# Performance work log

Measured on AMD Instinct MI355X. Metric: run time of the kernel, lower is better.

## Reference

```python
import jax, jax.numpy as jnp
import numpy as np

B, N, DIM, H = 4, 3072, 768, 3  # N must be 48*64 per positional-encoding assert; H must be 3 per reshape constraint
HD = DIM // H               # 256
D = HD + 6                  # per-head dim after positional concat


def _positional(n):
    # (x^2, y^2, xy, x, y, 1) encoding over a 48x64 grid, intrinsics=None path.
    h, w = 48, 64
    ys = jnp.linspace(-1.0, 1.0, h)
    xs = jnp.linspace(-1.0, 1.0, w)
    p3 = jnp.tile(ys, w)            # [N], ys.unsqueeze(0).repeat(B, w)
    p4 = jnp.repeat(xs, h)          # [N], xs.repeat_interleave(h)
    pos = jnp.stack([p3 * p3, p4 * p4, p3 * p4, p3, p4, jnp.ones_like(p3)], axis=-1)  # [N,6]
    return pos


def setup_inputs() -> dict:
    key = jax.random.key(0)
    k0, k1, k2 = jax.random.split(key, 3)
    x = jax.random.normal(k0, (B, N, DIM), dtype=jnp.float32)
    W_qkv = jax.random.normal(k1, (3 * DIM, DIM), dtype=jnp.float32) * (DIM ** -0.5)
    W_pf = jax.random.normal(k2, (DIM, DIM + 6 * H), dtype=jnp.float32) * ((DIM + 6 * H) ** -0.5)
    b_pf = jnp.zeros((DIM,), dtype=jnp.float32)
    return {"x": x, "W_qkv": W_qkv, "W_pf": W_pf, "b_pf": b_pf}


def reference(x, W_qkv, W_pf, b_pf):
    Bb, Nn, C = x.shape
    scale = HD ** -0.5
    qkv = (x @ W_qkv.T).reshape(Bb, Nn, 3, H, HD).transpose(2, 0, 3, 1, 4)  # [3,B,H,N,hd]
    q, k, v = qkv[0], qkv[1], qkv[2]
    attn = jnp.einsum('bhnd,bhmd->bhnm', q, k) * scale          # [B,H,N,N]
    attn_f = jax.nn.softmax(attn, axis=-1) * jax.nn.softmax(attn, axis=-2)
    pos = _positional(Nn)                                       # [N,6]
    pos_b = jnp.broadcast_to(pos[None, None], (Bb, H, Nn, 6))
    v_cat = jnp.concatenate([v, pos_b], axis=-1)                # [B,H,N,D]
    # fundamental = v^T @ attn_f @ v  -> [B,H,D,D]
    f1 = jnp.einsum('bhnd,bhnm->bhdm', v_cat, attn_f)
    fund = jnp.einsum('bhdm,bhme->bhde', f1, v_cat)
    # reshape [B,H,D,D] -> [B, 3D, D] -> transpose -> [B, D, 3D]
    fund = fund.reshape(Bb, H * D, D).transpose(0, 2, 1)
    out = fund @ W_pf.T + b_pf                                  # [B, D, DIM]
    return out
```

## Files before the change

### kernel.cpp

```cpp
#include <hip/hip_runtime.h>

typedef unsigned short u16;
typedef u16 u16x8 __attribute__((ext_vector_type(8)));
typedef u16 u16x4 __attribute__((ext_vector_type(4)));
typedef __bf16 bf16x8 __attribute__((ext_vector_type(8)));
typedef float f32x4 __attribute__((ext_vector_type(4)));

#define Bn   4
#define Nn   3072
#define DIMn 768
#define Hn   3
#define HDn  256
#define BHn  12
#define Dn   262
#define EP   272
#define MSn  8
#define FP   264
#define KSn  4

__device__ __forceinline__ u16 f2bf(float f) {
    unsigned u = __builtin_bit_cast(unsigned, f);
    u += 0x7fffu + ((u >> 16) & 1u);
    return (u16)(u >> 16);
}
__device__ __forceinline__ float bf2f(u16 h) {
    unsigned u = ((unsigned)h) << 16;
    return __builtin_bit_cast(float, u);
}
__device__ __forceinline__ bf16x8 ld_frag16(const u16* p) {
    return *(const bf16x8*)p;
}
#define MFMA(a,b,c) __builtin_amdgcn_mfma_f32_16x16x32_bf16(a, b, c, 0, 0, 0)

__global__ void to_bf16(const float* __restrict__ in, u16* __restrict__ out, int n8) {
    int i = blockIdx.x * blockDim.x + threadIdx.x;
    if (i >= n8) return;
    float4 a = *(const float4*)(in + (size_t)i*8);
    float4 b = *(const float4*)(in + (size_t)i*8 + 4);
    u16x8 o;
    o[0]=f2bf(a.x); o[1]=f2bf(a.y); o[2]=f2bf(a.z); o[3]=f2bf(a.w);
    o[4]=f2bf(b.x); o[5]=f2bf(b.y); o[6]=f2bf(b.z); o[7]=f2bf(b.w);
    *(u16x8*)(out + (size_t)i*8) = o;
}

__global__ __launch_bounds__(256) void transpose_wpf(const float* __restrict__ Wpf,
                                                     float* __restrict__ WpfT) {
    __shared__ float tile[32][33];
    int jt = blockIdx.x * 32;
    int ot = blockIdx.y * 32;
    int tx = threadIdx.x & 31, ty = threadIdx.x >> 5;
    #pragma unroll
    for (int k = 0; k < 4; ++k) {
        int o = ot + ty + 8*k;
        int j = jt + tx;
        tile[ty + 8*k][tx] = (j < 786) ? Wpf[(size_t)o*786 + j] : 0.0f;
    }
    __syncthreads();
    #pragma unroll
    for (int k = 0; k < 4; ++k) {
        int j = jt + ty + 8*k;
        if (j < 786) WpfT[(size_t)j*768 + ot + tx] = tile[tx][ty + 8*k];
    }
}

__global__ __launch_bounds__(256) void qkv_mfma(const u16* __restrict__ xb,
                                                const u16* __restrict__ Wb,
                                                u16* __restrict__ qh,
                                                u16* __restrict__ kh,
                                                u16* __restrict__ vT) {
    __shared__ u16 Pool[2*128*72];
    u16* Xs = Pool;
    u16* Ws = Pool + 128*72;
    int tid = threadIdx.x;
    int w = tid >> 6, lane = tid & 63, quad = lane >> 4, l15 = lane & 15;
    int lid = blockIdx.x + 18*blockIdx.y;
    int swz = (lid & 7)*216 + (lid >> 3);
    int cb = swz % 18, rb = swz / 18;
    int r0 = rb * 128;
    int b_ = rb / 24;
    int n0 = (rb % 24) * 128;
    int which = cb / 6;
    int c0l = (cb % 6) * 128;
    int h = c0l >> 8, hd0 = c0l & 255;
    int bh = b_ * Hn + h;
    int wr = w >> 1, wc = w & 1;
    const u16* xp = xb + (size_t)r0*DIMn;
    const u16* wp = Wb + (size_t)(which*768 + c0l)*DIMn;
    const int sr = tid >> 3, ssg = tid & 7;

    u16x8 xreg[4], wreg[4];
    #pragma unroll
    for (int i = 0; i < 4; ++i) {
        xreg[i] = *(const u16x8*)(xp + (size_t)(sr + 32*i)*DIMn + ssg*8);
        wreg[i] = *(const u16x8*)(wp + (size_t)(sr + 32*i)*DIMn + ssg*8);
    }

    f32x4 acc[4][4];
    #pragma unroll
    for (int i = 0; i < 4; ++i)
        #pragma unroll
        for (int j = 0; j < 4; ++j) acc[i][j] = (f32x4){0.f,0.f,0.f,0.f};

    for (int k0 = 0; k0 < DIMn; k0 += 64) {
        int k0n = (k0 + 64 < DIMn) ? k0 + 64 : 0;
        __syncthreads();
        #pragma unroll
        for (int i = 0; i < 4; ++i) {
            *(u16x8*)&Xs[(sr + 32*i)*72 + ssg*8] = xreg[i];
            *(u16x8*)&Ws[(sr + 32*i)*72 + ssg*8] = wreg[i];
        }
        __syncthreads();
        #pragma unroll
        for (int i = 0; i < 4; ++i) {
            xreg[i] = *(const u16x8*)(xp + (size_t)(sr + 32*i)*DIMn + k0n + ssg*8);
            wreg[i] = *(const u16x8*)(wp + (size_t)(sr + 32*i)*DIMn + k0n + ssg*8);
        }
        #pragma unroll
        for (int ks = 0; ks < 2; ++ks) {
            bf16x8 af[4], bf[4];
            #pragma unroll
            for (int mt = 0; mt < 4; ++mt)
                af[mt] = ld_frag16(&Xs[(wr*64 + mt*16 + l15)*72 + ks*32 + quad*8]);
            #pragma unroll
            for (int nt = 0; nt < 4; ++nt)
                bf[nt] = ld_frag16(&Ws[(wc*64 + nt*16 + l15)*72 + ks*32 + quad*8]);
            #pragma unroll
            for (int mt = 0; mt < 4; ++mt)
                #pragma unroll
                for (int nt = 0; nt < 4; ++nt)
                    acc[mt][nt] = MFMA(af[mt], bf[nt], acc[mt][nt]);
        }
    }
    __syncthreads();
    u16* Cw = Pool + w*(64*72);
    if (which < 2) {
        #pragma unroll
        for (int mt = 0; mt < 4; ++mt)
            #pragma unroll
            for (int nt = 0; nt < 4; ++nt)
                #pragma unroll
                for (int r = 0; r < 4; ++r)
                    Cw[(mt*16 + quad*4 + r)*72 + nt*16 + l15] = f2bf(acc[mt][nt][r]);
    } else {
        #pragma unroll
        for (int mt = 0; mt < 4; ++mt)
            #pragma unroll
            for (int nt = 0; nt < 4; ++nt) {
                u16x4 pk;
                #pragma unroll
                for (int r = 0; r < 4; ++r) pk[r] = f2bf(acc[mt][nt][r]);
                *(u16x4*)&Cw[(nt*16 + l15)*72 + mt*16 + quad*4] = pk;
            }
    }
    __syncthreads();
    #pragma unroll
    for (int i = 0; i < 8; ++i) {
        int u = tid + i*256;
        int row = u >> 4, seg = u & 15;
        if (which < 2) {
            int wv = ((row >> 6) << 1) | (seg >> 3);
            u16x8 vv = *(const u16x8*)&Pool[wv*(64*72) + (row & 63)*72 + (seg & 7)*8];
            u16* dst = (which == 0) ? qh : kh;
            *(u16x8*)(dst + ((size_t)bh*Nn + n0 + row)*HDn + hd0 + seg*8) = vv;
        } else {
            int wv = ((seg >> 3) << 1) | (row >> 6);
            u16x8 vv = *(const u16x8*)&Pool[wv*(64*72) + (row & 63)*72 + (seg & 7)*8];
            *(u16x8*)(vT + ((size_t)bh*EP + hd0 + row)*Nn + n0 + seg*8) = vv;
        }
    }
}

__global__ void pos_fill(u16* __restrict__ vT) {
    int idx = blockIdx.x * blockDim.x + threadIdx.x;
    int bh = idx / (16*Nn);
    int rem = idx - bh*16*Nn;
    int row = rem / Nn;
    int n = rem - row*Nn;
    int gy = n % 48, gx = n / 48;
    float p3 = -1.0f + (2.0f/47.0f)*gy;
    float p4 = -1.0f + (2.0f/63.0f)*gx;
    float v = 0.f;
    if (row == 0) v = p3*p3;
    else if (row == 1) v = p4*p4;
    else if (row == 2) v = p3*p4;
    else if (row == 3) v = p3;
    else if (row == 4) v = p4;
    else if (row == 5) v = 1.0f;
    vT[((size_t)bh*EP + 256 + row)*Nn + n] = f2bf(v);
}

__global__ __launch_bounds__(256) void rc_mfma(const u16* __restrict__ qh,
                                               const u16* __restrict__ kh,
                                               float* __restrict__ R_part,
                                               float* __restrict__ C_part,
                                               u16* __restrict__ P2,
                                               int g0) {
    __shared__ u16 Ks[64*264];
    __shared__ float rbuf[2][2][64];
    int tid = threadIdx.x;
    int w = tid >> 6, lane = tid & 63, quad = lane >> 4, l15 = lane & 15;
    int nwg = (int)(gridDim.x * gridDim.y * gridDim.z);
    int lid = blockIdx.x + (int)gridDim.x*(blockIdx.y + (int)gridDim.y*blockIdx.z);
    int swz = (lid & 7)*(nwg >> 3) + (lid >> 3);
    int ms = swz % MSn;
    int rem_ = swz / MSn;
    int nb = rem_ % 48;
    int bhl = rem_ / 48;
    int bh = g0 + bhl;
    int n0 = nb * 64;
    int msBase = ms * (Nn/MSn);
    const u16* qp = qh + ((size_t)bh*Nn + n0)*HDn;
    const u16* kp = kh + (size_t)bh*Nn*HDn;
    u16* pw = P2 + (size_t)bhl*Nn*Nn;
    int wm = w & 1, wn = w >> 1;

    #pragma unroll
    for (int i = 0; i < 8; ++i) {
        int e = tid + i*256;
        int row = e >> 5, seg = e & 31;
        *(u16x8*)&Ks[row*264 + seg*8] = *(const u16x8*)(qp + (size_t)row*HDn + seg*8);
    }
    __syncthreads();
    bf16x8 qf[2][8];
    #pragma unroll
    for (int nt = 0; nt < 2; ++nt)
        #pragma unroll
        for (int ks = 0; ks < 8; ++ks)
            qf[nt][ks] = ld_frag16(&Ks[((2*wn+nt)*16 + l15)*264 + ks*32 + quad*8]);

    const int kr = tid >> 5, ksg = tid & 31;
    u16x8 kreg[8];
    #pragma unroll
    for (int i = 0; i < 8; ++i)
        kreg[i] = *(const u16x8*)(kp + (size_t)(msBase + kr + 8*i)*HDn + ksg*8);

    float* cpart = C_part + ((size_t)(nb*2 + wn)*BHn + bh)*Nn;
    float rAcc[2] = {0.f, 0.f};
    const int NCH = Nn/(MSn*64);
    for (int mc = 0; mc < NCH; ++mc) {
        int m0 = msBase + mc*64;
        int m0n = msBase + ((mc + 1 < NCH) ? (mc + 1)*64 : 0);
        __syncthreads();
        #pragma unroll
        for (int i = 0; i < 8; ++i)
            *(u16x8*)&Ks[(kr + 8*i)*264 + ksg*8] = kreg[i];
        __syncthreads();
        #pragma unroll
        for (int i = 0; i < 8; ++i)
            kreg[i] = *(const u16x8*)(kp + (size_t)(m0n + kr + 8*i)*HDn + ksg*8);
        f32x4 sacc[2][2];
        #pragma unroll
        for (int i = 0; i < 2; ++i)
            #pragma unroll
            for (int j = 0; j < 2; ++j) sacc[i][j] = (f32x4){0.f,0.f,0.f,0.f};
        #pragma unroll
        for (int ks = 0; ks < 8; ++ks) {
            bf16x8 a0 = ld_frag16(&Ks[((2*wm+0)*16 + l15)*264 + ks*32 + quad*8]);
            bf16x8 a1 = ld_frag16(&Ks[((2*wm+1)*16 + l15)*264 + ks*32 + quad*8]);
            sacc[0][0] = MFMA(a0, qf[0][ks], sacc[0][0]);
            sacc[0][1] = MFMA(a0, qf[1][ks], sacc[0][1]);
            sacc[1][0] = MFMA(a1, qf[0][ks], sacc[1][0]);
            sacc[1][1] = MFMA(a1, qf[1][ks], sacc[1][1]);
        }
        float ex[2][2][4];
        #pragma unroll
        for (int mt = 0; mt < 2; ++mt)
            #pragma unroll
            for (int nt = 0; nt < 2; ++nt)
                #pragma unroll
                for (int r = 0; r < 4; ++r)
                    ex[mt][nt][r] = __expf(0.0625f * sacc[mt][nt][r]);
        #pragma unroll
        for (int mt = 0; mt < 2; ++mt)
            #pragma unroll
            for (int nt = 0; nt < 2; ++nt) {
                u16x4 pk;
                #pragma unroll
                for (int r = 0; r < 4; ++r) {
                    float e2 = ex[mt][nt][r];
                    pk[r] = f2bf(e2 * e2);
                }
                *(u16x4*)(pw + (size_t)(n0 + (2*wn+nt)*16 + l15)*Nn
                             + m0 + (2*wm+mt)*16 + quad*4) = pk;
            }
        #pragma unroll
        for (int nt = 0; nt < 2; ++nt)
            #pragma unroll
            for (int mt = 0; mt < 2; ++mt)
                #pragma unroll
                for (int r = 0; r < 4; ++r) rAcc[nt] += ex[mt][nt][r];
        {
            float v0 = ex[0][0][0] + ex[0][1][0];
            float v1 = ex[0][0][1] + ex[0][1][1];
            float v2 = ex[0][0][2] + ex[0][1][2];
            float v3 = ex[0][0][3] + ex[0][1][3];
            float v4 = ex[1][0][0] + ex[1][1][0];
            float v5 = ex[1][0][1] + ex[1][1][1];
            float v6 = ex[1][0][2] + ex[1][1][2];
            float v7 = ex[1][0][3] + ex[1][1][3];
            int b0 = l15 & 1, b1 = l15 & 2, b2 = l15 & 4;
            float u01 = (b0 ? v1 : v0) + __shfl_xor(b0 ? v0 : v1, 1, 16);
            float u23 = (b0 ? v3 : v2) + __shfl_xor(b0 ? v2 : v3, 1, 16);
            float u45 = (b0 ? v5 : v4) + __shfl_xor(b0 ? v4 : v5, 1, 16);
            float u67 = (b0 ? v7 : v6) + __shfl_xor(b0 ? v6 : v7, 1, 16);
            float t03 = (b1 ? u23 : u01) + __shfl_xor(b1 ? u01 : u23, 2, 16);
            float t47 = (b1 ? u67 : u45) + __shfl_xor(b1 ? u45 : u67, 2, 16);
            float s07 = (b2 ? t47 : t03) + __shfl_xor(b2 ? t03 : t47, 4, 16);
            s07 += __shfl_xor(s07, 8, 16);
            if (l15 < 8)
                cpart[m0 + (2*wm + (l15 >> 2))*16 + quad*4 + (l15 & 3)] = s07;
        }
    }
    #pragma unroll
    for (int nt = 0; nt < 2; ++nt) {
        float rp = rAcc[nt];
        rp += __shfl_xor(rp, 16, 64);
        rp += __shfl_xor(rp, 32, 64);
        if (quad == 0) rbuf[wm][nt][wn*32 + l15] = rp;
    }
    __syncthreads();
    #pragma unroll
    for (int nt = 0; nt < 2; ++nt) {
        if (quad == 0 && wm == 0) {
            float tot = rbuf[0][nt][wn*32 + l15] + rbuf[1][nt][wn*32 + l15];
            R_part[(size_t)ms*BHn*Nn + (size_t)bh*Nn + n0 + (2*wn+nt)*16 + l15] = tot;
        }
    }
}

__global__ void inv_kernel(const float* __restrict__ Rg,
                           const float* __restrict__ Cg,
                           float* __restrict__ iRg, float* __restrict__ iCg) {
    int i = blockIdx.x * blockDim.x + threadIdx.x;
    float r = 0.f;
    #pragma unroll
    for (int s = 0; s < MSn; ++s)
        r += Rg[(size_t)s*BHn*Nn + i];
    float c = 0.f;
    for (int s = 0; s < 96; ++s)
        c += Cg[(size_t)s*BHn*Nn + i];
    iRg[i] = 1.0f / r;
    iCg[i] = 1.0f / c;
}

__global__ void scale_v(const u16* __restrict__ vTg, const float* __restrict__ iCg,
                        u16* __restrict__ vTs) {
    int idx = blockIdx.x * blockDim.x + threadIdx.x;
    int bhl = idx / (EP*Nn/8);
    int rem = idx - bhl*(EP*Nn/8);
    size_t off = (size_t)bhl*EP*Nn + (size_t)rem*8;
    int m = (rem % (Nn/8)) * 8;
    u16x8 v = *(const u16x8*)(vTg + off);
    float4 c0 = *(const float4*)(iCg + (size_t)bhl*Nn + m);
    float4 c1 = *(const float4*)(iCg + (size_t)bhl*Nn + m + 4);
    u16x8 o;
    o[0]=f2bf(bf2f(v[0])*c0.x); o[1]=f2bf(bf2f(v[1])*c0.y);
    o[2]=f2bf(bf2f(v[2])*c0.z); o[3]=f2bf(bf2f(v[3])*c0.w);
    o[4]=f2bf(bf2f(v[4])*c1.x); o[5]=f2bf(bf2f(v[5])*c1.y);
    o[6]=f2bf(bf2f(v[6])*c1.z); o[7]=f2bf(bf2f(v[7])*c1.w);
    *(u16x8*)(vTs + off) = o;
}

__global__ __launch_bounds__(256, 4) void pv_mfma(const u16* __restrict__ P2,
                                                  const u16* __restrict__ vTs,
                                                  const float* __restrict__ iRg,
                                                  u16* __restrict__ f1aTg) {
    __shared__ u16 Ps2[64*72];
    __shared__ u16 Vt[144*72];
    int tid = threadIdx.x;
    int w = tid >> 6, lane = tid & 63, quad = lane >> 4, l15 = lane & 15;
    int nwg = (int)(gridDim.x * gridDim.y * gridDim.z);
    int lid = blockIdx.x + (int)gridDim.x*(blockIdx.y + (int)gridDim.y*blockIdx.z);
    int swz = (lid & 7)*(nwg >> 3) + (lid >> 3);
    int n0b = swz % 48;
    int rem_ = swz / 48;
    int bhl = rem_ % (int)gridDim.y;
    int z = rem_ / (int)gridDim.y;
    int n0 = n0b * 64;
    const u16* pp = P2  + ((size_t)bhl*Nn + n0)*Nn;
    const u16* vp = vTs + (size_t)bhl*EP*Nn + (size_t)(z*128)*Nn;
    const int sr = tid >> 3, sg = tid & 7;
    u16x8 preg[2], vreg[5];
    #pragma unroll
    for (int i = 0; i < 2; ++i)
        preg[i] = *(const u16x8*)(pp + (size_t)(sr + 32*i)*Nn + sg*8);
    #pragma unroll
    for (int i = 0; i < 5; ++i)
        if (i < 4 || (z == 1 && tid < 128))
            vreg[i] = *(const u16x8*)(vp + (size_t)(sr + 32*i)*Nn + sg*8);

    f32x4 acc[4][3];
    #pragma unroll
    for (int a = 0; a < 4; ++a)
        #pragma unroll
        for (int b = 0; b < 3; ++b) acc[a][b] = (f32x4){0.f,0.f,0.f,0.f};

    for (int mc = 0; mc < Nn/64; ++mc) {
        int m0n = (mc + 1 < Nn/64) ? (mc + 1)*64 : 0;
        __syncthreads();
        #pragma unroll
        for (int i = 0; i < 2; ++i)
            *(u16x8*)&Ps2[(sr + 32*i)*72 + sg*8] = preg[i];
        #pragma unroll
        for (int i = 0; i < 5; ++i)
            if (i < 4 || (z == 1 && tid < 128))
                *(u16x8*)&Vt[(sr + 32*i)*72 + sg*8] = vreg[i];
        __syncthreads();
        #pragma unroll
        for (int i = 0; i < 2; ++i)
            preg[i] = *(const u16x8*)(pp + (size_t)(sr + 32*i)*Nn + m0n + sg*8);
        #pragma unroll
        for (int i = 0; i < 5; ++i)
            if (i < 4 || (z == 1 && tid < 128))
                vreg[i] = *(const u16x8*)(vp + (size_t)(sr + 32*i)*Nn + m0n + sg*8);
        #pragma unroll
        for (int ks = 0; ks < 2; ++ks) {
            bf16x8 pa[4];
            #pragma unroll
            for (int nt = 0; nt < 4; ++nt)
                pa[nt] = ld_frag16(&Ps2[(nt*16 + l15)*72 + ks*32 + quad*8]);
            #pragma unroll
            for (int et = 0; et < 3; ++et) {
                const int lt = (et < 2) ? (w*2 + et) : 8;
                const bool act = (et < 2 || (z == 1 && w == 3));
                if (act) {
                    bf16x8 vb = ld_frag16(&Vt[(lt*16 + l15)*72 + ks*32 + quad*8]);
                    #pragma unroll
                    for (int nt = 0; nt < 4; ++nt)
                        acc[nt][et] = MFMA(pa[nt], vb, acc[nt][et]);
                }
            }
        }
    }
    #pragma unroll
    for (int nt = 0; nt < 4; ++nt) {
        float4 ir4 = *(const float4*)(iRg + (size_t)bhl*Nn + n0 + nt*16 + quad*4);
        #pragma unroll
        for (int et = 0; et < 3; ++et) {
            const int tile = (et < 2) ? (z*8 + w*2 + et) : 16;
            const bool act = (et < 2 || (z == 1 && w == 3));
            if (act) {
                int e = tile*16 + l15;
                u16x4 ov;
                #pragma unroll
                for (int r = 0; r < 4; ++r)
                    ov[r] = f2bf(acc[nt][et][r] * ((const float*)&ir4)[r]);
                *(u16x4*)(f1aTg + ((size_t)bhl*EP + e)*Nn + n0 + nt*16 + quad*4) = ov;
            }
        }
    }
}

__global__ __launch_bounds__(256) void fund_mfma(const u16* __restrict__ vT,
                                                 const u16* __restrict__ f1aT,
                                                 float* __restrict__ fund_part) {
    __shared__ u16 At[64*136];
    __shared__ u16 Bt[64*136];
    int tid = threadIdx.x;
    int w = tid >> 6, lane = tid & 63, quad = lane >> 4, l15 = lane & 15;
    int lid = blockIdx.x + 5*(blockIdx.y + 5*blockIdx.z);
    int swz = (lid & 7)*150 + (lid >> 3);
    int ex_ = swz % 5;
    int rem_ = swz / 5;
    int dx_ = rem_ % 5;
    int bz = rem_ / 5;
    int bh = bz >> 2;
    int ks = bz & 3;
    int d0 = dx_ * 64, e0 = ex_ * 64;
    const u16* ap = vT   + (size_t)bh*EP*Nn;
    const u16* bp = f1aT + (size_t)bh*EP*Nn;
    int wd = w & 1, we = w >> 1;
    const u16x8 zero8 = {0,0,0,0,0,0,0,0};
    const int nc0 = ks * (Nn/KSn);
    const int NCH = (Nn/KSn)/128;

    const int srow = tid >> 4, seg = tid & 15;
    u16x8 areg[4], breg[4];
    #pragma unroll
    for (int i = 0; i < 4; ++i) {
        int row = srow + 16*i;
        int da = d0 + row, eb = e0 + row;
        areg[i] = (da < EP) ? *(const u16x8*)(ap + (size_t)da*Nn + nc0 + seg*8) : zero8;
        breg[i] = (eb < EP) ? *(const u16x8*)(bp + (size_t)eb*Nn + nc0 + seg*8) : zero8;
    }

    f32x4 acc[2][2];
    #pragma unroll
    for (int i = 0; i < 2; ++i)
        #pragma unroll
        for (int j = 0; j < 2; ++j) acc[i][j] = (f32x4){0.f,0.f,0.f,0.f};

    for (int mc = 0; mc < NCH; ++mc) {
        int ncn = nc0 + ((mc + 1 < NCH) ? (mc + 1)*128 : 0);
        __syncthreads();
        #pragma unroll
        for (int i = 0; i < 4; ++i) {
            int row = srow + 16*i;
            *(u16x8*)&At[row*136 + seg*8] = areg[i];
            *(u16x8*)&Bt[row*136 + seg*8] = breg[i];
        }
        __syncthreads();
        #pragma unroll
        for (int i = 0; i < 4; ++i) {
            int row = srow + 16*i;
            int da = d0 + row, eb = e0 + row;
            areg[i] = (da < EP) ? *(const u16x8*)(ap + (size_t)da*Nn + ncn + seg*8) : zero8;
            breg[i] = (eb < EP) ? *(const u16x8*)(bp + (size_t)eb*Nn + ncn + seg*8) : zero8;
        }
        #pragma unroll
        for (int kk = 0; kk < 4; ++kk) {
            bf16x8 a0 = ld_frag16(&At[((2*wd+0)*16 + l15)*136 + kk*32 + quad*8]);
            bf16x8 a1 = ld_frag16(&At[((2*wd+1)*16 + l15)*136 + kk*32 + quad*8]);
            bf16x8 b0 = ld_frag16(&Bt[((2*we+0)*16 + l15)*136 + kk*32 + quad*8]);
            bf16x8 b1 = ld_frag16(&Bt[((2*we+1)*16 + l15)*136 + kk*32 + quad*8]);
            acc[0][0] = MFMA(a0, b0, acc[0][0]);
            acc[0][1] = MFMA(a0, b1, acc[0][1]);
            acc[1][0] = MFMA(a1, b0, acc[1][0]);
            acc[1][1] = MFMA(a1, b1, acc[1][1]);
        }
    }
    float* fp = fund_part + (size_t)(ks*BHn + bh)*Dn*FP;
    #pragma unroll
    for (int dt = 0; dt < 2; ++dt)
        #pragma unroll
        for (int et = 0; et < 2; ++et)
            #pragma unroll
            for (int r = 0; r < 4; ++r) {
                int d = d0 + (2*wd+dt)*16 + quad*4 + r;
                int e = e0 + (2*we+et)*16 + l15;
                if (d < Dn && e < Dn)
                    fp[(size_t)d*FP + e] = acc[dt][et][r];
            }
}

__device__ __forceinline__ float4 ld4sum(const float* p, size_t SL) {
    float4 a = *(const float4*)p;
    float4 b = *(const float4*)(p + SL);
    float4 c = *(const float4*)(p + 2*SL);
    float4 d = *(const float4*)(p + 3*SL);
    return (float4){a.x+b.x+c.x+d.x, a.y+b.y+c.y+d.y,
                    a.z+b.z+c.z+d.z, a.w+b.w+c.w+d.w};
}

__global__ __launch_bounds__(256) void out_gemm(const float* __restrict__ fund_part,
                                                const float* __restrict__ WpfT,
                                                const float* __restrict__ bpf,
                                                float* __restrict__ out) {
    __shared__ float As[2][16][68];
    __shared__ float Bs[2][16][68];
    const size_t SL = (size_t)BHn*Dn*FP;
    int tid = threadIdx.x;
    int b_ = blockIdx.z;
    int d2b = blockIdx.y * 64, ob = blockIdx.x * 64;
    int ty = tid >> 4, tx = tid & 15;
    int srow = tid >> 4, sc4 = (tid & 15) * 4;
    const int NIT = (786 + 15) / 16;

    float4 aReg, bReg;
    {
        int j = srow;
        int h = j / Dn, d1 = j - h*Dn;
        const float* srcA = fund_part + ((size_t)(b_*Hn + h)*Dn + d1)*FP + d2b + sc4;
        if (d2b + sc4 + 3 < Dn) aReg = ld4sum(srcA, SL);
        else {
            float t[4] = {0.f,0.f,0.f,0.f};
            for (int u2 = 0; u2 < 4; ++u2)
                if (d2b + sc4 + u2 < Dn)
                    t[u2] = srcA[u2] + srcA[u2+SL] + srcA[u2+2*SL] + srcA[u2+3*SL];
            aReg = (float4){t[0],t[1],t[2],t[3]};
        }
        bReg = *(const float4*)(WpfT + (size_t)j*768 + ob + sc4);
    }
    *(float4*)&As[0][srow][sc4] = aReg;
    *(float4*)&Bs[0][srow][sc4] = bReg;
    __syncthreads();

    float acc[4][4] = {};
    for (int c = 0; c < NIT; ++c) {
        int buf = c & 1;
        if (c + 1 < NIT) {
            int j = (c + 1)*16 + srow;
            aReg = (float4){0.f,0.f,0.f,0.f};
            bReg = (float4){0.f,0.f,0.f,0.f};
            if (j < 786) {
                int h = j / Dn, d1 = j - h*Dn;
                const float* srcA = fund_part + ((size_t)(b_*Hn + h)*Dn + d1)*FP + d2b + sc4;
                if (d2b + sc4 + 3 < Dn) aReg = ld4sum(srcA, SL);
                else {
                    float t[4] = {0.f,0.f,0.f,0.f};
                    for (int u2 = 0; u2 < 4; ++u2)
                        if (d2b + sc4 + u2 < Dn)
                            t[u2] = srcA[u2] + srcA[u2+SL] + srcA[u2+2*SL] + srcA[u2+3*SL];
                    aReg = (float4){t[0],t[1],t[2],t[3]};
                }
                bReg = *(const float4*)(WpfT + (size_t)j*768 + ob + sc4);
            }
        }
        #pragma unroll
        for (int kk = 0; kk < 16; ++kk) {
            float4 a = *(const float4*)&As[buf][kk][ty*4];
            float4 b = *(const float4*)&Bs[buf][kk][tx*4];
            acc[0][0] += a.x*b.x; acc[0][1] += a.x*b.y; acc[0][2] += a.x*b.z; acc[0][3] += a.x*b.w;
            acc[1][0] += a.y*b.x; acc[1][1] += a.y*b.y; acc[1][2] += a.y*b.z; acc[1][3] += a.y*b.w;
            acc[2][0] += a.z*b.x; acc[2][1] += a.z*b.y; acc[2][2] += a.z*b.z; acc[2][3] += a.z*b.w;
            acc[3][0] += a.w*b.x; acc[3][1] += a.w*b.y; acc[3][2] += a.w*b.z; acc[3][3] += a.w*b.w;
        }
        if (c + 1 < NIT) {
            *(float4*)&As[buf^1][srow][sc4] = aReg;
            *(float4*)&Bs[buf^1][srow][sc4] = bReg;
            __syncthreads();
        }
    }
    #pragma unroll
    for (int i = 0; i < 4; ++i) {
        int d2 = d2b + ty*4 + i;
        if (d2 >= Dn) continue;
        #pragma unroll
        for (int j = 0; j < 4; ++j) {
            int o = ob + tx*4 + j;
            out[((size_t)b_*Dn + d2)*DIMn + o] = acc[i][j] + bpf[o];
        }
    }
}

extern "C" void kernel_launch(void* const* d_in, const int* in_sizes, int n_in,
                              void* d_out, int out_size, void* d_ws, size_t ws_size,
                              hipStream_t stream) {
    const float* x    = (const float*)d_in[0];
    const float* Wqkv = (const float*)d_in[1];
    const float* Wpf  = (const float*)d_in[2];
    const float* bpf  = (const float*)d_in[3];
    float* out = (float*)d_out;

    char* p = (char*)d_ws;
    u16* qh    = (u16*)p;                       p += (size_t)BHn*Nn*HDn*2;
    u16* kh    = (u16*)p;                       p += (size_t)BHn*Nn*HDn*2;
    u16* vT    = (u16*)p;                       p += (size_t)BHn*EP*Nn*2;
    u16* f1aT  = (u16*)p;                       p += (size_t)BHn*EP*Nn*2;
    float* Cp  = (float*)p;                     p += (size_t)96*BHn*Nn*4;
    float* iR  = (float*)p;                     p += (size_t)BHn*Nn*4;
    float* iC  = (float*)p;                     p += (size_t)BHn*Nn*4;
    float* fund= (float*)p;                     p += (size_t)KSn*BHn*Dn*FP*4 + 256;
    float* WpfT= (float*)p;                     p += (size_t)786*768*4;
    char* region2 = p;
    size_t fixedB = (size_t)(region2 - (char*)d_ws);
    size_t avail = (ws_size > fixedB) ? (ws_size - fixedB) : 0;

    const size_t perBh = ((size_t)Nn*Nn + (size_t)EP*Nn) * 2;
    const size_t rpB   = (size_t)MSn*BHn*Nn*4;
    int gbh = 1;
    const int cand[5] = {12, 6, 4, 3, 2};
    for (int ci = 0; ci < 5; ++ci) {
        if ((size_t)cand[ci]*perBh + rpB <= avail) { gbh = cand[ci]; break; }
    }

    u16* xb = (u16*)region2;
    u16* Wb = xb + (size_t)Bn*Nn*DIMn;
    u16* P2  = (u16*)region2;
    u16* vTs = P2 + (size_t)gbh*Nn*Nn;
    float* Rp = (float*)(vTs + (size_t)gbh*EP*Nn);

    to_bf16  <<<dim3((Bn*Nn*DIMn/8 + 255)/256), 256, 0, stream>>>(x, xb, Bn*Nn*DIMn/8);
    to_bf16  <<<dim3((3*DIMn*DIMn/8 + 255)/256), 256, 0, stream>>>(Wqkv, Wb, 3*DIMn*DIMn/8);
    transpose_wpf<<<dim3(25, 24), 256, 0, stream>>>(Wpf, WpfT);
    qkv_mfma <<<dim3(18, 96), 256, 0, stream>>>(xb, Wb, qh, kh, vT);
    pos_fill <<<dim3(BHn*16*Nn/256), 256, 0, stream>>>(vT);

    for (int g0 = 0; g0 < BHn; g0 += gbh) {
        rc_mfma  <<<dim3(MSn, Nn/64, gbh), 256, 0, stream>>>(qh, kh, Rp, Cp, P2, g0);
        inv_kernel<<<dim3(gbh*Nn/256), 256, 0, stream>>>(
            Rp + (size_t)g0*Nn, Cp + (size_t)g0*Nn, iR + (size_t)g0*Nn, iC + (size_t)g0*Nn);
        scale_v  <<<dim3(gbh*EP*Nn/8/256), 256, 0, stream>>>(
            vT + (size_t)g0*EP*Nn, iC + (size_t)g0*Nn, vTs);
        pv_mfma  <<<dim3(Nn/64, gbh, 2), 256, 0, stream>>>(
            P2, vTs, iR + (size_t)g0*Nn, f1aT + (size_t)g0*EP*Nn);
    }

    fund_mfma<<<dim3(5, 5, BHn*KSn), 256, 0, stream>>>(vT, f1aT, fund);
    out_gemm <<<dim3(DIMn/64, 5, Bn), 256, 0, stream>>>(fund, WpfT, bpf, out);
}
```

Before: 498.1 us.

## Double Q rows per rc_mfma block to reuse each K tile twice

Each rc_mfma workgroup now handles 128 query rows instead of 64, keeping two sets of Q fragments in registers and running twice the MFMAs per K tile loaded into shared memory. This halves how often K is streamed from global memory and cuts the grid size in half. The C_part slices are indexed by nb*4+sn*2+wn, so the 96 partial column sums read by inv_kernel still line up. The cost is higher register pressure (32 Q fragments plus 8 accumulators), which may lower occupancy, and fewer workgroups for the GPU to spread across its compute units.

```diff
diff --git a/kernel.cpp b/kernel.cpp
--- a/kernel.cpp
+++ b/kernel.cpp
@@ -196,7 +196,7 @@
                                                u16* __restrict__ P2,
                                                int g0) {
     __shared__ u16 Ks[64*264];
-    __shared__ float rbuf[2][2][64];
+    __shared__ float rbuf[2][2][2][64];
     int tid = threadIdx.x;
     int w = tid >> 6, lane = tid & 63, quad = lane >> 4, l15 = lane & 15;
     int nwg = (int)(gridDim.x * gridDim.y * gridDim.z);
@@ -204,38 +204,42 @@
     int swz = (lid & 7)*(nwg >> 3) + (lid >> 3);
     int ms = swz % MSn;
     int rem_ = swz / MSn;
-    int nb = rem_ % 48;
-    int bhl = rem_ / 48;
+    int nb = rem_ % 24;
+    int bhl = rem_ / 24;
     int bh = g0 + bhl;
-    int n0 = nb * 64;
+    int n0 = nb * 128;
     int msBase = ms * (Nn/MSn);
     const u16* qp = qh + ((size_t)bh*Nn + n0)*HDn;
     const u16* kp = kh + (size_t)bh*Nn*HDn;
     u16* pw = P2 + (size_t)bhl*Nn*Nn;
     int wm = w & 1, wn = w >> 1;
 
-    #pragma unroll
-    for (int i = 0; i < 8; ++i) {
-        int e = tid + i*256;
-        int row = e >> 5, seg = e & 31;
-        *(u16x8*)&Ks[row*264 + seg*8] = *(const u16x8*)(qp + (size_t)row*HDn + seg*8);
-    }
-    __syncthreads();
-    bf16x8 qf[2][8];
-    #pragma unroll
-    for (int nt = 0; nt < 2; ++nt)
-        #pragma unroll
-        for (int ks = 0; ks < 8; ++ks)
-            qf[nt][ks] = ld_frag16(&Ks[((2*wn+nt)*16 + l15)*264 + ks*32 + quad*8]);
-
     const int kr = tid >> 5, ksg = tid & 31;
     u16x8 kreg[8];
     #pragma unroll
     for (int i = 0; i < 8; ++i)
         kreg[i] = *(const u16x8*)(kp + (size_t)(msBase + kr + 8*i)*HDn + ksg*8);
 
-    float* cpart = C_part + ((size_t)(nb*2 + wn)*BHn + bh)*Nn;
-    float rAcc[2] = {0.f, 0.f};
+    bf16x8 qf[2][2][8];
+    #pragma unroll
+    for (int p = 0; p < 2; ++p) {
+        if (p) __syncthreads();
+        #pragma unroll
+        for (int i = 0; i < 8; ++i) {
+            int e = tid + i*256;
+            int row = e >> 5, seg = e & 31;
+            *(u16x8*)&Ks[row*264 + seg*8] =
+                *(const u16x8*)(qp + (size_t)(p*64 + row)*HDn + seg*8);
+        }
+        __syncthreads();
+        #pragma unroll
+        for (int nt = 0; nt < 2; ++nt)
+            #pragma unroll
+            for (int ks = 0; ks < 8; ++ks)
+                qf[p][nt][ks] = ld_frag16(&Ks[((2*wn+nt)*16 + l15)*264 + ks*32 + quad*8]);
+    }
+
+    float rAcc[2][2] = {{0.f,0.f},{0.f,0.f}};
     const int NCH = Nn/(MSn*64);
     for (int mc = 0; mc < NCH; ++mc) {
         int m0 = msBase + mc*64;
@@ -248,84 +252,104 @@
         #pragma unroll
         for (int i = 0; i < 8; ++i)
             kreg[i] = *(const u16x8*)(kp + (size_t)(m0n + kr + 8*i)*HDn + ksg*8);
-        f32x4 sacc[2][2];
+        f32x4 s0[2][2], s1[2][2];
         #pragma unroll
         for (int i = 0; i < 2; ++i)
             #pragma unroll
-            for (int j = 0; j < 2; ++j) sacc[i][j] = (f32x4){0.f,0.f,0.f,0.f};
+            for (int j = 0; j < 2; ++j) {
+                s0[i][j] = (f32x4){0.f,0.f,0.f,0.f};
+                s1[i][j] = (f32x4){0.f,0.f,0.f,0.f};
+            }
         #pragma unroll
         for (int ks = 0; ks < 8; ++ks) {
             bf16x8 a0 = ld_frag16(&Ks[((2*wm+0)*16 + l15)*264 + ks*32 + quad*8]);
             bf16x8 a1 = ld_frag16(&Ks[((2*wm+1)*16 + l15)*264 + ks*32 + quad*8]);
-            sacc[0][0] = MFMA(a0, qf[0][ks], sacc[0][0]);
-            sacc[0][1] = MFMA(a0, qf[1][ks], sacc[0][1]);
-            sacc[1][0] = MFMA(a1, qf[0][ks], sacc[1][0]);
-            sacc[1][1] = MFMA(a1, qf[1][ks], sacc[1][1]);
-        }
-        float ex[2][2][4];
-        #pragma unroll
-        for (int mt = 0; mt < 2; ++mt)
+            s0[0][0] = MFMA(a0, qf[0][0][ks], s0[0][0]);
+            s0[0][1] = MFMA(a0, qf[0][1][ks], s0[0][1]);
+            s0[1][0] = MFMA(a1, qf[0][0][ks], s0[1][0]);
+            s0[1][1] = MFMA(a1, qf[0][1][ks], s0[1][1]);
+            s1[0][0] = MFMA(a0, qf[1][0][ks], s1[0][0]);
+            s1[0][1] = MFMA(a0, qf[1][1][ks], s1[0][1]);
+            s1[1][0] = MFMA(a1, qf[1][0][ks], s1[1][0]);
+            s1[1][1] = MFMA(a1, qf[1][1][ks], s1[1][1]);
+        }
+        #pragma unroll
+        for (int sn = 0; sn < 2; ++sn) {
+            float ex[2][2][4];
+            #pragma unroll
+            for (int mt = 0; mt < 2; ++mt)
+                #pragma unroll
+                for (int nt = 0; nt < 2; ++nt)
+                    #pragma unroll
+                    for (int r = 0; r < 4; ++r) {
+                        float sv = sn ? s1[mt][nt][r] : s0[mt][nt][r];
+                        ex[mt][nt][r] = __expf(0.0625f * sv);
+                    }
+            #pragma unroll
+            for (int mt = 0; mt < 2; ++mt)
+                #pragma unroll
+                for (int nt = 0; nt < 2; ++nt) {
+                    u16x4 pk;
+                    #pragma unroll
+                    for (int r = 0; r < 4; ++r) {
+                        float e2 = ex[mt][nt][r];
+                        pk[r] = f2bf(e2 * e2);
+                    }
+                    *(u16x4*)(pw + (size_t)(n0 + sn*64 + (2*wn+nt)*16 + l15)*Nn
+                                 + m0 + (2*wm+mt)*16 + quad*4) = pk;
+                }
             #pragma unroll
             for (int nt = 0; nt < 2; ++nt)
                 #pragma unroll
-                for (int r = 0; r < 4; ++r)
-                    ex[mt][nt][r] = __expf(0.0625f * sacc[mt][nt][r]);
-        #pragma unroll
-        for (int mt = 0; mt < 2; ++mt)
-            #pragma unroll
-            for (int nt = 0; nt < 2; ++nt) {
-                u16x4 pk;
-                #pragma unroll
-                for (int r = 0; r < 4; ++r) {
-                    float e2 = ex[mt][nt][r];
-                    pk[r] = f2bf(e2 * e2);
+                for (int mt = 0; mt < 2; ++mt)
+                    #pragma unroll
+                    for (int r = 0; r < 4; ++r) rAcc[sn][nt] += ex[mt][nt][r];
+            {
+                float v0 = ex[0][0][0] + ex[0][1][0];
+                float v1 = ex[0][0][1] + ex[0][1][1];
+                float v2 = ex[0][0][2] + ex[0][1][2];
+                float v3 = ex[0][0][3] + ex[0][1][3];
+                float v4 = ex[1][0][0] + ex[1][1][0];
+                float v5 = ex[1][0][1] + ex[1][1][1];
+                float v6 = ex[1][0][2] + ex[1][1][2];
+                float v7 = ex[1][0][3] + ex[1][1][3];
+                int b0 = l15 & 1, b1 = l15 & 2, b2 = l15 & 4;
+                float u01 = (b0 ? v1 : v0) + __shfl_xor(b0 ? v0 : v1, 1, 16);
+                float u23 = (b0 ? v3 : v2) + __shfl_xor(b0 ? v2 : v3, 1, 16);
+                float u45 = (b0 ? v5 : v4) + __shfl_xor(b0 ? v4 : v5, 1, 16);
+                float u67 = (b0 ? v7 : v6) + __shfl_xor(b0 ? v6 : v7, 1, 16);
+                float t03 = (b1 ? u23 : u01) + __shfl_xor(b1 ? u01 : u23, 2, 16);
+                float t47 = (b1 ? u67 : u45) + __shfl_xor(b1 ? u45 : u67, 2, 16);
+                float s07 = (b2 ? t47 : t03) + __shfl_xor(b2 ? t03 : t47, 4, 16);
+                s07 += __shfl_xor(s07, 8, 16);
+                if (l15 < 8) {
+                    float* cpart = C_part
+                        + ((size_t)(nb*4 + sn*2 + wn)*BHn + bh)*Nn;
+                    cpart[m0 + (2*wm + (l15 >> 2))*16 + quad*4 + (l15 & 3)] = s07;
                 }
-                *(u16x4*)(pw + (size_t)(n0 + (2*wn+nt)*16 + l15)*Nn
-                             + m0 + (2*wm+mt)*16 + quad*4) = pk;
             }
-        #pragma unroll
-        for (int nt = 0; nt < 2; ++nt)
-            #pragma unroll
-            for (int mt = 0; mt < 2; ++mt)
-                #pragma unroll
-                for (int r = 0; r < 4; ++r) rAcc[nt] += ex[mt][nt][r];
-        {
-            float v0 = ex[0][0][0] + ex[0][1][0];
-            float v1 = ex[0][0][1] + ex[0][1][1];
-            float v2 = ex[0][0][2] + ex[0][1][2];
-            float v3 = ex[0][0][3] + ex[0][1][3];
-            float v4 = ex[1][0][0] + ex[1][1][0];
-            float v5 = ex[1][0][1] + ex[1][1][1];
-            float v6 = ex[1][0][2] + ex[1][1][2];
-            float v7 = ex[1][0][3] + ex[1][1][3];
-            int b0 = l15 & 1, b1 = l15 & 2, b2 = l15 & 4;
-            float u01 = (b0 ? v1 : v0) + __shfl_xor(b0 ? v0 : v1, 1, 16);
-            float u23 = (b0 ? v3 : v2) + __shfl_xor(b0 ? v2 : v3, 1, 16);
-            float u45 = (b0 ? v5 : v4) + __shfl_xor(b0 ? v4 : v5, 1, 16);
-            float u67 = (b0 ? v7 : v6) + __shfl_xor(b0 ? v6 : v7, 1, 16);
-            float t03 = (b1 ? u23 : u01) + __shfl_xor(b1 ? u01 : u23, 2, 16);
-            float t47 = (b1 ? u67 : u45) + __shfl_xor(b1 ? u45 : u67, 2, 16);
-            float s07 = (b2 ? t47 : t03) + __shfl_xor(b2 ? t03 : t47, 4, 16);
-            s07 += __shfl_xor(s07, 8, 16);
-            if (l15 < 8)
-                cpart[m0 + (2*wm + (l15 >> 2))*16 + quad*4 + (l15 & 3)] = s07;
-        }
-    }
-    #pragma unroll
-    for (int nt = 0; nt < 2; ++nt) {
-        float rp = rAcc[nt];
-        rp += __shfl_xor(rp, 16, 64);
-        rp += __shfl_xor(rp, 32, 64);
-        if (quad == 0) rbuf[wm][nt][wn*32 + l15] = rp;
-    }
+        }
+    }
+    #pragma unroll
+    for (int sn = 0; sn < 2; ++sn)
+        #pragma unroll
+        for (int nt = 0; nt < 2; ++nt) {
+            float rp = rAcc[sn][nt];
+            rp += __shfl_xor(rp, 16, 64);
+            rp += __shfl_xor(rp, 32, 64);
+            if (quad == 0) rbuf[sn][wm][nt][wn*32 + l15] = rp;
+        }
     __syncthreads();
     #pragma unroll
-    for (int nt = 0; nt < 2; ++nt) {
-        if (quad == 0 && wm == 0) {
-            float tot = rbuf[0][nt][wn*32 + l15] + rbuf[1][nt][wn*32 + l15];
-            R_part[(size_t)ms*BHn*Nn + (size_t)bh*Nn + n0 + (2*wn+nt)*16 + l15] = tot;
-        }
-    }
+    for (int sn = 0; sn < 2; ++sn)
+        #pragma unroll
+        for (int nt = 0; nt < 2; ++nt) {
+            if (quad == 0 && wm == 0) {
+                float tot = rbuf[sn][0][nt][wn*32 + l15] + rbuf[sn][1][nt][wn*32 + l15];
+                R_part[(size_t)ms*BHn*Nn + (size_t)bh*Nn
+                       + n0 + sn*64 + (2*wn+nt)*16 + l15] = tot;
+            }
+        }
 }
 
 __global__ void inv_kernel(const float* __restrict__ Rg,
@@ -667,7 +691,7 @@
     pos_fill <<<dim3(BHn*16*Nn/256), 256, 0, stream>>>(vT);
 
     for (int g0 = 0; g0 < BHn; g0 += gbh) {
-        rc_mfma  <<<dim3(MSn, Nn/64, gbh), 256, 0, stream>>>(qh, kh, Rp, Cp, P2, g0);
+        rc_mfma  <<<dim3(MSn, Nn/128, gbh), 256, 0, stream>>>(qh, kh, Rp, Cp, P2, g0);
         inv_kernel<<<dim3(gbh*Nn/256), 256, 0, stream>>>(
             Rp + (size_t)g0*Nn, Cp + (size_t)g0*Nn, iR + (size_t)g0*Nn, iC + (size_t)g0*Nn);
         scale_v  <<<dim3(gbh*EP*Nn/8/256), 256, 0, stream>>>(
```

New measurement: 531.8 us. 1.07x slower.
